# Kernel optimization log

Hardware: AMD Instinct MI355X
Metric: run time of the kernel (lower is better)

## Reference

```python
import jax, jax.numpy as jnp
import numpy as np

B, D = 8192, 1024
HR, HE, HF = 512, 4096, 2048
N_OPS, N_TASKS = 4, 4

def setup_inputs() -> dict:
    key = jax.random.key(0)
    ks = jax.random.split(key, 20)
    s = 0.02
    return {
        "x":        jax.random.normal(ks[0], (B, D), jnp.float32),
        # router
        "W_r1":   s*jax.random.normal(ks[1], (D, HR), jnp.float32),
        "b_r1":     jnp.zeros((HR,), jnp.float32),
        "W_dom":  s*jax.random.normal(ks[2], (HR, 2), jnp.float32),
        "b_dom":    jnp.zeros((2,), jnp.float32),
        "W_mop":  s*jax.random.normal(ks[3], (HR, N_OPS), jnp.float32),
        "W_lt":   s*jax.random.normal(ks[4], (HR, N_TASKS), jnp.float32),
        # math expert (operation hint = additive embedding)
        "op_emb": s*jax.random.normal(ks[5], (N_OPS, D), jnp.float32),
        "W_m1":   s*jax.random.normal(ks[6], (D, HE), jnp.float32),
        "b_m1":     jnp.zeros((HE,), jnp.float32),
        "W_m2":   s*jax.random.normal(ks[7], (HE, D), jnp.float32),
        "b_m2":     jnp.zeros((D,), jnp.float32),
        # language expert (task hint = additive embedding)
        "task_emb": s*jax.random.normal(ks[8], (N_TASKS, D), jnp.float32),
        "W_l1":   s*jax.random.normal(ks[9], (D, HE), jnp.float32),
        "b_l1":     jnp.zeros((HE,), jnp.float32),
        "W_l2":   s*jax.random.normal(ks[10], (HE, D), jnp.float32),
        "b_l2":     jnp.zeros((D,), jnp.float32),
        # fusion
        "W_f1":   s*jax.random.normal(ks[11], (D, HF), jnp.float32),
        "b_f1":     jnp.zeros((HF,), jnp.float32),
        "W_f2":   s*jax.random.normal(ks[12], (HF, D), jnp.float32),
        "b_f2":     jnp.zeros((D,), jnp.float32),
    }

def reference(x, W_r1, b_r1, W_dom, b_dom, W_mop, W_lt,
              op_emb, W_m1, b_m1, W_m2, b_m2,
              task_emb, W_l1, b_l1, W_l2, b_l2,
              W_f1, b_f1, W_f2, b_f2):
    # --- router ---
    h = jax.nn.relu(x @ W_r1 + b_r1)                      # [B, HR]
    dom_logits = h @ W_dom + b_dom                        # [B, 2]
    expert_weights = jax.nn.softmax(dom_logits, axis=-1)  # [B, 2]
    primary = jnp.argmax(dom_logits, axis=-1)             # [B]
    math_op = jnp.argmax(h @ W_mop, axis=-1)              # [B]
    lang_task = jnp.argmax(h @ W_lt, axis=-1)             # [B]
    # --- experts (vectorized equivalent of per-sample dispatch) ---
    math_in = x + op_emb[math_op]                         # [B, D]
    math_out = jax.nn.relu(math_in @ W_m1 + b_m1) @ W_m2 + b_m2
    lang_in = x + task_emb[lang_task]                     # [B, D]
    lang_out = jax.nn.relu(lang_in @ W_l1 + b_l1) @ W_l2 + b_l2
    selected = jnp.where((primary == 0)[:, None], math_out, lang_out)  # [B, D]
    # --- fusion: scale by routing weight of the chosen expert + MLP residual ---
    w = jnp.take_along_axis(expert_weights, primary[:, None], axis=1)  # [B, 1]
    fused = w * selected
    final = fused + jax.nn.relu(fused @ W_f1 + b_f1) @ W_f2 + b_f2     # [B, D]
    return final
```

## Files before the change

kernel.cpp:

```cpp
#include <hip/hip_runtime.h>
#include <hip/hip_bf16.h>
#include <stdint.h>

#define NB 8192
#define DD 1024
#define HRD 512
#define HED 4096
#define HFD 2048

typedef __attribute__((ext_vector_type(8))) short bf16x8;
typedef __attribute__((ext_vector_type(4))) float f32x4;
typedef unsigned short u16;

__device__ __forceinline__ u16 f2b(float f) {
    union { float f; uint32_t i; } c; c.f = f;
    uint32_t r = c.i + 0x7FFF + ((c.i >> 16) & 1);
    return (u16)(r >> 16);
}
__device__ __forceinline__ float b2f(u16 u) {
    union { uint32_t i; float f; } c; c.i = ((uint32_t)u) << 16; return c.f;
}

__device__ __forceinline__ void xcd_swz(int flat, int nwg, int nFast, int& f, int& s) {
    int xcd = flat & 7, rest = flat >> 3;
    int q = nwg >> 3, r = nwg & 7;
    int wg = (xcd < r ? xcd * (q + 1) : r * (q + 1) + (xcd - r) * q) + rest;
    f = wg % nFast; s = wg / nFast;
}

#define GLDS(g, l) __builtin_amdgcn_global_load_lds( \
    (const __attribute__((address_space(1))) void*)(g), \
    (__attribute__((address_space(3))) void*)(l), 16, 0, 0)

__global__ void k_init(int* cnt) { if (threadIdx.x < 2) cnt[threadIdx.x] = 0; }

__global__ __launch_bounds__(256) void k_split(const float4* __restrict__ x4,
                                               ushort4* __restrict__ hi4,
                                               ushort4* __restrict__ lo4) {
    int i = blockIdx.x * 256 + threadIdx.x;
    float4 v = x4[i];
    ushort4 h, l;
    h.x = f2b(v.x); l.x = f2b(v.x - b2f(h.x));
    h.y = f2b(v.y); l.y = f2b(v.y - b2f(h.y));
    h.z = f2b(v.z); l.z = f2b(v.z - b2f(h.z));
    h.w = f2b(v.w); l.w = f2b(v.w - b2f(h.w));
    hi4[i] = h; lo4[i] = l;
}

__global__ __launch_bounds__(256) void k_transpose(const float* __restrict__ in,
                                                   u16* __restrict__ out, int R, int C) {
    __shared__ float s[64][65];
    int tx = threadIdx.x & 63, ty = threadIdx.x >> 6;
    int c0 = blockIdx.x * 64, r0 = blockIdx.y * 64;
#pragma unroll
    for (int j = 0; j < 16; j++) { int r = ty + j * 4; s[r][tx] = in[(size_t)(r0 + r) * C + c0 + tx]; }
    __syncthreads();
#pragma unroll
    for (int j = 0; j < 16; j++) { int c = ty + j * 4; out[(size_t)(c0 + c) * R + r0 + tx] = f2b(s[tx][c]); }
}

__global__ __launch_bounds__(256) void k_transpose_split(const float* __restrict__ in,
                                                         u16* __restrict__ ohi, u16* __restrict__ olo,
                                                         int R, int C) {
    __shared__ float s[64][65];
    int tx = threadIdx.x & 63, ty = threadIdx.x >> 6;
    int c0 = blockIdx.x * 64, r0 = blockIdx.y * 64;
#pragma unroll
    for (int j = 0; j < 16; j++) { int r = ty + j * 4; s[r][tx] = in[(size_t)(r0 + r) * C + c0 + tx]; }
    __syncthreads();
#pragma unroll
    for (int j = 0; j < 16; j++) {
        int c = ty + j * 4;
        float v = s[tx][c];
        u16 h = f2b(v);
        ohi[(size_t)(c0 + c) * R + r0 + tx] = h;
        olo[(size_t)(c0 + c) * R + r0 + tx] = f2b(v - b2f(h));
    }
}

__device__ __forceinline__ void stage_tile(const char* gRowBase, long rowStrideBytes,
                                           u16* s, int tid) {
    int wave = tid >> 6, lane = tid & 63;
#pragma unroll
    for (int is = 0; is < 4; ++is) {
        int c = wave * 4 + is;
        int row = c * 8 + (lane >> 3);
        const char* g = gRowBase + (long)row * rowStrideBytes + (lane & 7) * 16;
        GLDS(g, (char*)s + c * 1024);
    }
}

__global__ __launch_bounds__(256) void k_router(const u16* __restrict__ Ah, const u16* __restrict__ Al,
                                                const u16* __restrict__ Bh, const u16* __restrict__ Bl,
                                                const float* __restrict__ bias, float* __restrict__ H) {
    __shared__ u16 sAh[2][128 * 64], sAl[2][128 * 64], sBh[2][128 * 64], sBl[2][128 * 64];
    int tid = threadIdx.x, lane = tid & 63, wave = tid >> 6;
    int flat = blockIdx.y * gridDim.x + blockIdx.x;
    int bm, bn;
    xcd_swz(flat, gridDim.x * gridDim.y, gridDim.y, bn, bm);
    f32x4 acc[4][4];
#pragma unroll
    for (int i = 0; i < 4; i++)
#pragma unroll
        for (int j = 0; j < 4; j++) acc[i][j] = (f32x4)0.f;
    int wm = (wave & 1) * 64, wn = (wave >> 1) * 64;
    const char* ahBase = (const char*)(Ah + (size_t)bm * 128 * DD);
    const char* alBase = (const char*)(Al + (size_t)bm * 128 * DD);
    const char* bhBase = (const char*)(Bh + (size_t)bn * 128 * DD);
    const char* blBase = (const char*)(Bl + (size_t)bn * 128 * DD);
    const int nk = DD / 64;
    stage_tile(ahBase, DD * 2, sAh[0], tid);
    stage_tile(alBase, DD * 2, sAl[0], tid);
    stage_tile(bhBase, DD * 2, sBh[0], tid);
    stage_tile(blBase, DD * 2, sBl[0], tid);
    asm volatile("s_waitcnt vmcnt(0)" ::: "memory");
    __builtin_amdgcn_s_barrier();
    int cur = 0;
    for (int it = 0; it < nk; ++it) {
        if (it + 1 < nk) {
            size_t ofs = (size_t)(it + 1) * 128;
            stage_tile(ahBase + ofs, DD * 2, sAh[cur ^ 1], tid);
            stage_tile(alBase + ofs, DD * 2, sAl[cur ^ 1], tid);
            stage_tile(bhBase + ofs, DD * 2, sBh[cur ^ 1], tid);
            stage_tile(blBase + ofs, DD * 2, sBl[cur ^ 1], tid);
        }
        const u16* pAh = sAh[cur]; const u16* pAl = sAl[cur];
        const u16* pBh = sBh[cur]; const u16* pBl = sBl[cur];
#pragma unroll
        for (int kk = 0; kk < 2; kk++) {
            int kofs = kk * 64 + (lane >> 4) * 16;
            bf16x8 vbh[4], vbl[4];
#pragma unroll
            for (int ni = 0; ni < 4; ni++) {
                int rB = (wn + ni * 16 + (lane & 15)) * 128 + kofs;
                vbh[ni] = *(const bf16x8*)((const char*)pBh + rB);
                vbl[ni] = *(const bf16x8*)((const char*)pBl + rB);
            }
#pragma unroll
            for (int mi = 0; mi < 4; mi++) {
                int rA = (wm + mi * 16 + (lane & 15)) * 128 + kofs;
                bf16x8 vah = *(const bf16x8*)((const char*)pAh + rA);
                bf16x8 val = *(const bf16x8*)((const char*)pAl + rA);
#pragma unroll
                for (int ni = 0; ni < 4; ni++) {
                    acc[mi][ni] = __builtin_amdgcn_mfma_f32_16x16x32_bf16(vah, vbh[ni], acc[mi][ni], 0, 0, 0);
                    acc[mi][ni] = __builtin_amdgcn_mfma_f32_16x16x32_bf16(vah, vbl[ni], acc[mi][ni], 0, 0, 0);
                    acc[mi][ni] = __builtin_amdgcn_mfma_f32_16x16x32_bf16(val, vbh[ni], acc[mi][ni], 0, 0, 0);
                }
            }
        }
        asm volatile("s_waitcnt vmcnt(0)" ::: "memory");
        __builtin_amdgcn_s_barrier();
        cur ^= 1;
    }
    int quad = lane >> 4, cl = lane & 15;
#pragma unroll
    for (int mi = 0; mi < 4; mi++)
#pragma unroll
        for (int r = 0; r < 4; r++) {
            int row = bm * 128 + wm + mi * 16 + quad * 4 + r;
#pragma unroll
            for (int ni = 0; ni < 4; ni++) {
                int col = bn * 128 + wn + ni * 16 + cl;
                float v = acc[mi][ni][r] + bias[col];
                H[(size_t)row * HRD + col] = fmaxf(v, 0.f);
            }
        }
}

__global__ __launch_bounds__(256) void k_heads(const float* __restrict__ H,
                                               const float* __restrict__ Wd, const float* __restrict__ bd,
                                               const float* __restrict__ Wm, const float* __restrict__ Wl,
                                               int* __restrict__ cnt, int* __restrict__ perm,
                                               float* __restrict__ wsc, int* __restrict__ eic) {
    int lane = threadIdx.x & 63, wave = threadIdx.x >> 6;
    int r = blockIdx.x * 4 + wave;
    const float4* h4 = (const float4*)(H + (size_t)r * HRD);
    float4 v0 = h4[lane * 2], v1 = h4[lane * 2 + 1];
    float hv[8] = {v0.x, v0.y, v0.z, v0.w, v1.x, v1.y, v1.z, v1.w};
    float a[10];
#pragma unroll
    for (int t = 0; t < 10; t++) a[t] = 0.f;
    int kbase = lane * 8;
#pragma unroll
    for (int j = 0; j < 8; j++) {
        int k = kbase + j;
        float h_ = hv[j];
        float2 wd = ((const float2*)Wd)[k];
        a[0] += h_ * wd.x; a[1] += h_ * wd.y;
        float4 wm = ((const float4*)Wm)[k];
        a[2] += h_ * wm.x; a[3] += h_ * wm.y; a[4] += h_ * wm.z; a[5] += h_ * wm.w;
        float4 wl = ((const float4*)Wl)[k];
        a[6] += h_ * wl.x; a[7] += h_ * wl.y; a[8] += h_ * wl.z; a[9] += h_ * wl.w;
    }
#pragma unroll
    for (int t = 0; t < 10; t++)
#pragma unroll
        for (int off = 32; off > 0; off >>= 1) a[t] += __shfl_down(a[t], off);
    if (lane == 0) {
        float d0 = a[0] + bd[0], d1 = a[1] + bd[1];
        int primary = (d1 > d0) ? 1 : 0;
        float w = 1.f / (1.f + expf(-fabsf(d0 - d1)));
        int mi = 0; float mv = a[2];
        if (a[3] > mv) { mv = a[3]; mi = 1; }
        if (a[4] > mv) { mv = a[4]; mi = 2; }
        if (a[5] > mv) { mv = a[5]; mi = 3; }
        int li = 0; float lv = a[6];
        if (a[7] > lv) { lv = a[7]; li = 1; }
        if (a[8] > lv) { lv = a[8]; li = 2; }
        int pos;
        if (a[9] > lv) { lv = a[9]; li = 3; }
        if (primary == 0) pos = atomicAdd(&cnt[0], 1);
        else              pos = NB - 1 - atomicAdd(&cnt[1], 1);
        perm[pos] = r; wsc[pos] = w; eic[pos] = (primary == 0) ? mi : li;
    }
}

__global__ __launch_bounds__(256) void k_gather(const float* __restrict__ x,
                                                const float* __restrict__ op_emb,
                                                const float* __restrict__ task_emb,
                                                const int* __restrict__ perm, const int* __restrict__ eic,
                                                const int* __restrict__ cnt, u16* __restrict__ xin) {
    int lane = threadIdx.x & 63, wave = threadIdx.x >> 6;
    int i = blockIdx.x * 4 + wave;
    int n0 = cnt[0];
    int r = perm[i];
    const float* emb = ((i >= n0) ? task_emb : op_emb) + (size_t)eic[i] * DD;
    const float4* x4 = (const float4*)(x + (size_t)r * DD);
    const float4* e4 = (const float4*)emb;
    ushort4* o4 = (ushort4*)(xin + (size_t)i * DD);
#pragma unroll
    for (int j = 0; j < 4; j++) {
        int idx = lane + j * 64;
        float4 xv = x4[idx], ev = e4[idx];
        ushort4 o;
        o.x = f2b(xv.x + ev.x); o.y = f2b(xv.y + ev.y);
        o.z = f2b(xv.z + ev.z); o.w = f2b(xv.w + ev.w);
        o4[idx] = o;
    }
}

template <bool DUAL>
__global__ __launch_bounds__(512) void k_g256(
    const u16* __restrict__ A, const u16* __restrict__ B0w, const u16* __restrict__ B1w,
    const float* __restrict__ bias0, const float* __restrict__ bias1,
    u16* __restrict__ Out, int K, int N, const int* __restrict__ cnt) {
    __shared__ __align__(16) u16 sA[2][256 * 64];
    __shared__ __align__(16) u16 sB[2][256 * 64];
    const int tid = threadIdx.x, lane = tid & 63, wave = tid >> 6;
    int flat = blockIdx.y * gridDim.x + blockIdx.x;
    int t, bn;
    xcd_swz(flat, gridDim.x * gridDim.y, gridDim.y, bn, t);

    int tile = t, storeLo = 0, storeHi = 0x7fffffff;
    const u16* Bt = B0w; const float* bias = bias0;
    if constexpr (DUAL) {
        int n0 = cnt[0];
        int tb = n0 >> 8;
        bool isMath = (t <= tb) && (t < NB / 256);
        tile = isMath ? t : (t - 1);
        if (isMath) { storeLo = tile * 256; storeHi = n0 < storeLo + 256 ? n0 : storeLo + 256; }
        else        { storeHi = tile * 256 + 256; storeLo = n0 > tile * 256 ? n0 : tile * 256;
                      Bt = B1w; bias = bias1; }
        if (storeLo >= storeHi) return;
    }

    f32x4 acc[8][4];
#pragma unroll
    for (int i = 0; i < 8; i++)
#pragma unroll
        for (int j = 0; j < 4; j++) acc[i][j] = (f32x4)0.f;

    const int wm = (wave & 1) * 128;
    const int wn = (wave >> 1) * 64;
    const int rl = lane & 15, q = lane >> 4, x7 = lane & 7;
    const int aRow = (wave & 1) * 64;
    const int bRow = (wave >> 1) * 32;

    const long stride = (long)K * 2;
    const char* aBase = (const char*)A + (size_t)tile * 256 * stride;
    const char* bBase = (const char*)Bt + (size_t)bn * 256 * stride;
    const long srcOfs = (long)((lane & 7) ^ (lane >> 3)) << 4;
    const int waveOfs = wave * 1024;
    const int l8 = lane >> 3;

    auto SH_A = [&](int h, int kt, int d) {
        long kofs = (long)kt * 128 + srcOfs;
#pragma unroll
        for (int i = 0; i < 2; i++) {
            int gr = wave * 8 + l8 + h * 64 + i * 128;
            GLDS(aBase + (long)gr * stride + kofs,
                 (char*)&sA[d][0] + h * 16384 + i * 8192 + waveOfs);
        }
    };
    auto SH_B = [&](int h, int kt, int d) {
        long kofs = (long)kt * 128 + srcOfs;
#pragma unroll
        for (int i = 0; i < 2; i++) {
            int rp = i * 64 + wave * 8 + l8;
            int gn = (rp & 31) + ((rp >> 5) << 6) + h * 32;
            GLDS(bBase + (long)gn * stride + kofs,
                 (char*)&sB[d][0] + h * 16384 + i * 8192 + waveOfs);
        }
    };

    const int nk = K >> 6;
    SH_A(0, 0, 0); SH_B(0, 0, 0); SH_B(1, 0, 0); SH_A(1, 0, 0);
    if (nk > 1) {
        SH_A(0, 1, 1); SH_B(0, 1, 1); SH_B(1, 1, 1);
        asm volatile("s_waitcnt vmcnt(6)" ::: "memory");
    } else {
        asm volatile("s_waitcnt vmcnt(0)" ::: "memory");
    }
    __builtin_amdgcn_s_barrier();

    bf16x8 va[4][2], vb0[2][2], vb1[2][2];
    for (int kt = 0; kt < nk; ++kt) {
        const int cur = kt & 1;
        const char* pA = (const char*)&sA[cur][0];
        const char* pB = (const char*)&sB[cur][0];
#pragma unroll
        for (int f = 0; f < 4; f++)
#pragma unroll
            for (int kk = 0; kk < 2; kk++)
                va[f][kk] = *(const bf16x8*)(pA + (aRow + f * 16 + rl) * 128 + (((kk * 4 + q) ^ x7) << 4));
#pragma unroll
        for (int g = 0; g < 2; g++)
#pragma unroll
            for (int kk = 0; kk < 2; kk++)
                vb0[g][kk] = *(const bf16x8*)(pB + (bRow + g * 16 + rl) * 128 + (((kk * 4 + q) ^ x7) << 4));
        if (kt + 1 < nk) SH_A(1, kt + 1, cur ^ 1);
        __builtin_amdgcn_s_setprio(1);
#pragma unroll
        for (int f = 0; f < 4; f++)
#pragma unroll
            for (int g = 0; g < 2; g++)
#pragma unroll
                for (int kk = 0; kk < 2; kk++)
                    acc[f][g] = __builtin_amdgcn_mfma_f32_16x16x32_bf16(va[f][kk], vb0[g][kk], acc[f][g], 0, 0, 0);
        __builtin_amdgcn_s_setprio(0);
        asm volatile("" ::: "memory");
        __builtin_amdgcn_s_barrier();
#pragma unroll
        for (int g = 0; g < 2; g++)
#pragma unroll
            for (int kk = 0; kk < 2; kk++)
                vb1[g][kk] = *(const bf16x8*)(pB + (bRow + 128 + g * 16 + rl) * 128 + (((kk * 4 + q) ^ x7) << 4));
        if (kt + 2 < nk) SH_B(0, kt + 2, cur);
        __builtin_amdgcn_s_setprio(1);
#pragma unroll
        for (int f = 0; f < 4; f++)
#pragma unroll
            for (int g = 0; g < 2; g++)
#pragma unroll
                for (int kk = 0; kk < 2; kk++)
                    acc[f][2 + g] = __builtin_amdgcn_mfma_f32_16x16x32_bf16(va[f][kk], vb1[g][kk], acc[f][2 + g], 0, 0, 0);
        __builtin_amdgcn_s_setprio(0);
        asm volatile("" ::: "memory");
        __builtin_amdgcn_s_barrier();
#pragma unroll
        for (int f = 0; f < 4; f++)
#pragma unroll
            for (int kk = 0; kk < 2; kk++)
                va[f][kk] = *(const bf16x8*)(pA + (aRow + 128 + f * 16 + rl) * 128 + (((kk * 4 + q) ^ x7) << 4));
        if (kt + 2 < nk) SH_B(1, kt + 2, cur);
        __builtin_amdgcn_s_setprio(1);
#pragma unroll
        for (int f = 0; f < 4; f++)
#pragma unroll
            for (int g = 0; g < 2; g++)
#pragma unroll
                for (int kk = 0; kk < 2; kk++)
                    acc[4 + f][2 + g] = __builtin_amdgcn_mfma_f32_16x16x32_bf16(va[f][kk], vb1[g][kk], acc[4 + f][2 + g], 0, 0, 0);
        __builtin_amdgcn_s_setprio(0);
        asm volatile("" ::: "memory");
        __builtin_amdgcn_s_barrier();
        if (kt + 2 < nk) {
            SH_A(0, kt + 2, cur);
            asm volatile("s_waitcnt vmcnt(6)" ::: "memory");
        } else {
            asm volatile("s_waitcnt vmcnt(0)" ::: "memory");
        }
        __builtin_amdgcn_s_setprio(1);
#pragma unroll
        for (int f = 0; f < 4; f++)
#pragma unroll
            for (int g = 0; g < 2; g++)
#pragma unroll
                for (int kk = 0; kk < 2; kk++)
                    acc[4 + f][g] = __builtin_amdgcn_mfma_f32_16x16x32_bf16(va[f][kk], vb0[g][kk], acc[4 + f][g], 0, 0, 0);
        __builtin_amdgcn_s_setprio(0);
        asm volatile("" ::: "memory");
        __builtin_amdgcn_s_barrier();
    }

    const int quad = lane >> 4, cl = lane & 15;
#pragma unroll
    for (int f = 0; f < 8; f++)
#pragma unroll
        for (int rr = 0; rr < 4; rr++) {
            int grow = tile * 256 + wm + ((f & 3) * 16) + ((f >> 2) * 64) + quad * 4 + rr;
            if constexpr (DUAL) { if (grow < storeLo || grow >= storeHi) continue; }
#pragma unroll
            for (int g = 0; g < 4; g++) {
                int col = bn * 256 + wn + ((g & 1) * 16) + ((g >> 1) * 32) + cl;
                float v = acc[f][g][rr] + bias[col];
                Out[(size_t)grow * N + col] = f2b(fmaxf(v, 0.f));
            }
        }
}

template <int EPI, bool DUAL>
__global__ __launch_bounds__(512) void k_gemm8p(
    const u16* __restrict__ A, const u16* __restrict__ B0, const u16* __restrict__ B1,
    const float* __restrict__ bias0, const float* __restrict__ bias1,
    void* __restrict__ Out, int K, int N,
    const int* __restrict__ cnt, const float* __restrict__ wsel,
    const int* __restrict__ perm, const u16* __restrict__ resid) {
    __shared__ __align__(16) u16 sA[2][128 * 64];
    __shared__ __align__(16) u16 sB[2][128 * 64];
    const int tid = threadIdx.x, lane = tid & 63, wave = tid >> 6;
    int flat = blockIdx.y * gridDim.x + blockIdx.x;
    int t, bn;
    xcd_swz(flat, gridDim.x * gridDim.y, gridDim.y, bn, t);

    int n0 = 0, tile = t, storeLo = 0, storeHi = 0x7fffffff;
    const u16* Bt = B0; const float* bias = bias0;
    if constexpr (DUAL) {
        n0 = cnt[0];
        int tb = n0 >> 7;
        bool isMath = (t <= tb) && (t < 64);
        tile = isMath ? t : (t - 1);
        if (isMath) { storeLo = tile * 128; storeHi = n0 < storeLo + 128 ? n0 : storeLo + 128; }
        else        { storeHi = tile * 128 + 128; storeLo = n0 > tile * 128 ? n0 : tile * 128;
                      Bt = B1; bias = bias1; }
        if (storeLo >= storeHi) return;
    }

    f32x4 acc[4][2];
#pragma unroll
    for (int i = 0; i < 4; i++)
#pragma unroll
        for (int j = 0; j < 2; j++) acc[i][j] = (f32x4)0.f;

    const int wm = (wave & 1) * 64;
    const int wn = (wave >> 1) * 32;
    const int rl = lane & 15, q = lane >> 4, x7 = lane & 7;

    const long stride = (long)K * 2;
    const char* aBase = (const char*)A + (size_t)tile * 128 * stride;
    const char* bBase = (const char*)Bt + (size_t)bn * 128 * stride;
    const int rowInUnit = tid >> 3;
    const long srcOfs = (long)((tid & 7) ^ (rowInUnit & 7)) << 4;
    const int ldsWaveOfs = wave * 1024;

    auto STAGE = [&](int kt, int d) {
        long kofs = (long)kt * 128 + srcOfs;
#pragma unroll
        for (int i = 0; i < 2; i++)
            GLDS(aBase + (long)(i * 64 + rowInUnit) * stride + kofs,
                 (char*)&sA[d][0] + i * 8192 + ldsWaveOfs);
#pragma unroll
        for (int i = 0; i < 2; i++)
            GLDS(bBase + (long)(i * 64 + rowInUnit) * stride + kofs,
                 (char*)&sB[d][0] + i * 8192 + ldsWaveOfs);
    };

    STAGE(0, 0);
    const int nk = K >> 6;
    for (int k = 0; k < nk; ++k) {
        const int r_ = k & 1;
        if (k + 1 < nk) {
            STAGE(k + 1, r_ ^ 1);
            asm volatile("s_waitcnt vmcnt(4)" ::: "memory");
        } else {
            asm volatile("s_waitcnt vmcnt(0)" ::: "memory");
        }
        __builtin_amdgcn_s_barrier();
        const char* pA = (const char*)&sA[r_][0];
        const char* pB = (const char*)&sB[r_][0];
        bf16x8 vaA[2][2], vaB[2][2], vb0[2], vb1[2];
#pragma unroll
        for (int f = 0; f < 2; f++)
#pragma unroll
            for (int kk = 0; kk < 2; kk++)
                vaA[f][kk] = *(const bf16x8*)(pA + (wm + f * 16 + rl) * 128 + (((kk * 4 + q) ^ x7) << 4));
#pragma unroll
        for (int kk = 0; kk < 2; kk++)
            vb0[kk] = *(const bf16x8*)(pB + (wn + rl) * 128 + (((kk * 4 + q) ^ x7) << 4));
        __builtin_amdgcn_s_setprio(1);
#pragma unroll
        for (int f = 0; f < 2; f++)
#pragma unroll
            for (int kk = 0; kk < 2; kk++)
                acc[f][0] = __builtin_amdgcn_mfma_f32_16x16x32_bf16(vaA[f][kk], vb0[kk], acc[f][0], 0, 0, 0);
        __builtin_amdgcn_s_setprio(0);
#pragma unroll
        for (int kk = 0; kk < 2; kk++)
            vb1[kk] = *(const bf16x8*)(pB + (wn + 16 + rl) * 128 + (((kk * 4 + q) ^ x7) << 4));
        __builtin_amdgcn_s_setprio(1);
#pragma unroll
        for (int f = 0; f < 2; f++)
#pragma unroll
            for (int kk = 0; kk < 2; kk++)
                acc[f][1] = __builtin_amdgcn_mfma_f32_16x16x32_bf16(vaA[f][kk], vb1[kk], acc[f][1], 0, 0, 0);
        __builtin_amdgcn_s_setprio(0);
#pragma unroll
        for (int f = 0; f < 2; f++)
#pragma unroll
            for (int kk = 0; kk < 2; kk++)
                vaB[f][kk] = *(const bf16x8*)(pA + (wm + 32 + f * 16 + rl) * 128 + (((kk * 4 + q) ^ x7) << 4));
        __builtin_amdgcn_s_setprio(1);
#pragma unroll
        for (int f = 0; f < 2; f++)
#pragma unroll
            for (int kk = 0; kk < 2; kk++)
                acc[2 + f][1] = __builtin_amdgcn_mfma_f32_16x16x32_bf16(vaB[f][kk], vb1[kk], acc[2 + f][1], 0, 0, 0);
        __builtin_amdgcn_s_setprio(0);
        __builtin_amdgcn_s_setprio(1);
#pragma unroll
        for (int f = 0; f < 2; f++)
#pragma unroll
            for (int kk = 0; kk < 2; kk++)
                acc[2 + f][0] = __builtin_amdgcn_mfma_f32_16x16x32_bf16(vaB[f][kk], vb0[kk], acc[2 + f][0], 0, 0, 0);
        __builtin_amdgcn_s_setprio(0);
        asm volatile("" ::: "memory");
        __builtin_amdgcn_s_barrier();
    }

    const int quad = lane >> 4, cl = lane & 15;
#pragma unroll
    for (int mi = 0; mi < 4; mi++)
#pragma unroll
        for (int r = 0; r < 4; r++) {
            int grow = tile * 128 + wm + mi * 16 + quad * 4 + r;
            if constexpr (DUAL) { if (grow < storeLo || grow >= storeHi) continue; }
#pragma unroll
            for (int ni = 0; ni < 2; ni++) {
                int col = bn * 128 + wn + ni * 16 + cl;
                float v = acc[mi][ni][r] + bias[col];
                if constexpr (EPI == 0) {
                    ((u16*)Out)[(size_t)grow * N + col] = f2b(fmaxf(v, 0.f));
                } else if constexpr (EPI == 1) {
                    ((u16*)Out)[(size_t)grow * N + col] = f2b(v * wsel[grow]);
                } else {
                    v += b2f(resid[(size_t)grow * N + col]);
                    ((float*)Out)[(size_t)perm[grow] * N + col] = v;
                }
            }
        }
}

extern "C" void kernel_launch(void* const* d_in, const int* in_sizes, int n_in,
                              void* d_out, int out_size, void* d_ws, size_t ws_size,
                              hipStream_t stream) {
    const float* x      = (const float*)d_in[0];
    const float* W_r1   = (const float*)d_in[1];
    const float* b_r1   = (const float*)d_in[2];
    const float* W_dom  = (const float*)d_in[3];
    const float* b_dom  = (const float*)d_in[4];
    const float* W_mop  = (const float*)d_in[5];
    const float* W_lt   = (const float*)d_in[6];
    const float* op_emb = (const float*)d_in[7];
    const float* W_m1   = (const float*)d_in[8];
    const float* b_m1   = (const float*)d_in[9];
    const float* W_m2   = (const float*)d_in[10];
    const float* b_m2   = (const float*)d_in[11];
    const float* task_emb = (const float*)d_in[12];
    const float* W_l1   = (const float*)d_in[13];
    const float* b_l1   = (const float*)d_in[14];
    const float* W_l2   = (const float*)d_in[15];
    const float* b_l2   = (const float*)d_in[16];
    const float* W_f1   = (const float*)d_in[17];
    const float* b_f1   = (const float*)d_in[18];
    const float* W_f2   = (const float*)d_in[19];
    const float* b_f2   = (const float*)d_in[20];

    char* wsp = (char*)d_ws;
    size_t off = 0;
    auto take = [&](size_t bytes) -> char* {
        char* p = wsp + off;
        off += (bytes + 255) & ~(size_t)255;
        return p;
    };
    u16* Wr_hi = (u16*)take((size_t)HRD * DD * 2);
    u16* Wr_lo = (u16*)take((size_t)HRD * DD * 2);
    u16* Wm1t  = (u16*)take((size_t)HED * DD * 2);
    u16* Wl1t  = (u16*)take((size_t)HED * DD * 2);
    u16* Wm2t  = (u16*)take((size_t)DD * HED * 2);
    u16* Wl2t  = (u16*)take((size_t)DD * HED * 2);
    u16* Wf1t  = (u16*)take((size_t)HFD * DD * 2);
    u16* Wf2t  = (u16*)take((size_t)DD * HFD * 2);
    u16* x_hi  = (u16*)take((size_t)NB * DD * 2);
    u16* x_lo  = (u16*)take((size_t)NB * DD * 2);
    float* Hbuf = (float*)take((size_t)NB * HRD * 4);
    u16* hid   = (u16*)take((size_t)NB * HED * 2);
    int* cnt   = (int*)take(256);
    int* perm  = (int*)take(NB * 4);
    int* eic   = (int*)take(NB * 4);
    float* wsc = (float*)take(NB * 4);
    u16* xin   = x_hi;
    u16* fused = x_lo;
    u16* hid2  = Wm1t;

    k_init<<<1, 64, 0, stream>>>(cnt);
    k_split<<<(NB * DD / 4) / 256, 256, 0, stream>>>((const float4*)x, (ushort4*)x_hi, (ushort4*)x_lo);
    k_transpose_split<<<dim3(HRD / 64, DD / 64), 256, 0, stream>>>(W_r1, Wr_hi, Wr_lo, DD, HRD);
    k_transpose<<<dim3(HED / 64, DD / 64), 256, 0, stream>>>(W_m1, Wm1t, DD, HED);
    k_transpose<<<dim3(HED / 64, DD / 64), 256, 0, stream>>>(W_l1, Wl1t, DD, HED);
    k_transpose<<<dim3(DD / 64, HED / 64), 256, 0, stream>>>(W_m2, Wm2t, HED, DD);
    k_transpose<<<dim3(DD / 64, HED / 64), 256, 0, stream>>>(W_l2, Wl2t, HED, DD);
    k_transpose<<<dim3(HFD / 64, DD / 64), 256, 0, stream>>>(W_f1, Wf1t, DD, HFD);
    k_transpose<<<dim3(DD / 64, HFD / 64), 256, 0, stream>>>(W_f2, Wf2t, HFD, DD);

    k_router<<<dim3(NB / 128, HRD / 128), 256, 0, stream>>>(x_hi, x_lo, Wr_hi, Wr_lo, b_r1, Hbuf);
    k_heads<<<NB / 4, 256, 0, stream>>>(Hbuf, W_dom, b_dom, W_mop, W_lt, cnt, perm, wsc, eic);
    k_gather<<<NB / 4, 256, 0, stream>>>(x, op_emb, task_emb, perm, eic, cnt, xin);

    k_g256<true><<<dim3(NB / 256 + 1, HED / 256), 512, 0, stream>>>(
        xin, Wm1t, Wl1t, b_m1, b_l1, hid, DD, HED, cnt);
    k_gemm8p<1, true><<<dim3(NB / 128 + 1, DD / 128), 512, 0, stream>>>(
        hid, Wm2t, Wl2t, b_m2, b_l2, fused, HED, DD, cnt, wsc, nullptr, nullptr);
    k_g256<false><<<dim3(NB / 256, HFD / 256), 512, 0, stream>>>(
        fused, Wf1t, nullptr, b_f1, nullptr, hid2, DD, HFD, cnt);
    k_gemm8p<2, false><<<dim3(NB / 128, DD / 128), 512, 0, stream>>>(
        hid2, Wf2t, nullptr, b_f2, nullptr, d_out, HFD, DD, cnt, nullptr, perm, fused);
}
```

Baseline: 647.6 us.

## Use 256x128 tiles with staggered half-tile prefetch in down-projection GEMMs

Replaces the 128x128 double-buffered GEMM used for the expert down-projection and the fusion second layer with a 256x128 tile kernel. Global-to-LDS loads are split into A and B halves and issued between the four MFMA phases of each k-step, with barriers between phases. The aim is more reuse per B load and better overlap of memory traffic with matrix math. In exchange it uses more LDS and accumulator registers and launches half as many workgroups, which may lower occupancy and leave fewer blocks to spread across CUs.

```diff
diff --git a/kernel.cpp b/kernel.cpp
--- a/kernel.cpp
+++ b/kernel.cpp
@@ -411,118 +411,141 @@
 }
 
 template <int EPI, bool DUAL>
-__global__ __launch_bounds__(512) void k_gemm8p(
+__global__ __launch_bounds__(512) void k_gSTAG(
     const u16* __restrict__ A, const u16* __restrict__ B0, const u16* __restrict__ B1,
     const float* __restrict__ bias0, const float* __restrict__ bias1,
     void* __restrict__ Out, int K, int N,
     const int* __restrict__ cnt, const float* __restrict__ wsel,
     const int* __restrict__ perm, const u16* __restrict__ resid) {
-    __shared__ __align__(16) u16 sA[2][128 * 64];
+    __shared__ __align__(16) u16 sA[2][256 * 64];
     __shared__ __align__(16) u16 sB[2][128 * 64];
     const int tid = threadIdx.x, lane = tid & 63, wave = tid >> 6;
     int flat = blockIdx.y * gridDim.x + blockIdx.x;
     int t, bn;
     xcd_swz(flat, gridDim.x * gridDim.y, gridDim.y, bn, t);
 
-    int n0 = 0, tile = t, storeLo = 0, storeHi = 0x7fffffff;
+    int tile = t, storeLo = 0, storeHi = 0x7fffffff;
     const u16* Bt = B0; const float* bias = bias0;
     if constexpr (DUAL) {
-        n0 = cnt[0];
-        int tb = n0 >> 7;
-        bool isMath = (t <= tb) && (t < 64);
+        int n0 = cnt[0];
+        int tb = n0 >> 8;
+        bool isMath = (t <= tb) && (t < NB / 256);
         tile = isMath ? t : (t - 1);
-        if (isMath) { storeLo = tile * 128; storeHi = n0 < storeLo + 128 ? n0 : storeLo + 128; }
-        else        { storeHi = tile * 128 + 128; storeLo = n0 > tile * 128 ? n0 : tile * 128;
+        if (isMath) { storeLo = tile * 256; storeHi = n0 < storeLo + 256 ? n0 : storeLo + 256; }
+        else        { storeHi = tile * 256 + 256; storeLo = n0 > tile * 256 ? n0 : tile * 256;
                       Bt = B1; bias = bias1; }
         if (storeLo >= storeHi) return;
     }
 
-    f32x4 acc[4][2];
-#pragma unroll
-    for (int i = 0; i < 4; i++)
+    f32x4 acc[8][2];
+#pragma unroll
+    for (int i = 0; i < 8; i++)
 #pragma unroll
         for (int j = 0; j < 2; j++) acc[i][j] = (f32x4)0.f;
 
-    const int wm = (wave & 1) * 64;
+    const int wm = (wave & 1) * 128;
     const int wn = (wave >> 1) * 32;
     const int rl = lane & 15, q = lane >> 4, x7 = lane & 7;
+    const int aRow = (wave & 1) * 64;
+    const int bRow = (wave >> 1) * 16;
 
     const long stride = (long)K * 2;
-    const char* aBase = (const char*)A + (size_t)tile * 128 * stride;
+    const char* aBase = (const char*)A + (size_t)tile * 256 * stride;
     const char* bBase = (const char*)Bt + (size_t)bn * 128 * stride;
-    const int rowInUnit = tid >> 3;
-    const long srcOfs = (long)((tid & 7) ^ (rowInUnit & 7)) << 4;
-    const int ldsWaveOfs = wave * 1024;
-
-    auto STAGE = [&](int kt, int d) {
+    const long srcOfs = (long)((lane & 7) ^ (lane >> 3)) << 4;
+    const int waveOfs = wave * 1024;
+    const int l8 = lane >> 3;
+
+    auto SH_A = [&](int h, int kt, int d) {
         long kofs = (long)kt * 128 + srcOfs;
 #pragma unroll
-        for (int i = 0; i < 2; i++)
-            GLDS(aBase + (long)(i * 64 + rowInUnit) * stride + kofs,
-                 (char*)&sA[d][0] + i * 8192 + ldsWaveOfs);
-#pragma unroll
-        for (int i = 0; i < 2; i++)
-            GLDS(bBase + (long)(i * 64 + rowInUnit) * stride + kofs,
-                 (char*)&sB[d][0] + i * 8192 + ldsWaveOfs);
+        for (int i = 0; i < 2; i++) {
+            int gr = wave * 8 + l8 + h * 64 + i * 128;
+            GLDS(aBase + (long)gr * stride + kofs,
+                 (char*)&sA[d][0] + h * 16384 + i * 8192 + waveOfs);
+        }
     };
-
-    STAGE(0, 0);
+    auto SH_B = [&](int h, int kt, int d) {
+        long kofs = (long)kt * 128 + srcOfs;
+        int rp = wave * 8 + l8;
+        int gn = (rp & 15) + ((rp >> 4) << 5) + h * 16;
+        GLDS(bBase + (long)gn * stride + kofs,
+             (char*)&sB[d][0] + h * 8192 + waveOfs);
+    };
+
     const int nk = K >> 6;
-    for (int k = 0; k < nk; ++k) {
-        const int r_ = k & 1;
-        if (k + 1 < nk) {
-            STAGE(k + 1, r_ ^ 1);
+    SH_A(0, 0, 0); SH_B(0, 0, 0); SH_B(1, 0, 0); SH_A(1, 0, 0);
+    if (nk > 1) {
+        SH_A(0, 1, 1); SH_B(0, 1, 1); SH_B(1, 1, 1);
+        asm volatile("s_waitcnt vmcnt(4)" ::: "memory");
+    } else {
+        asm volatile("s_waitcnt vmcnt(0)" ::: "memory");
+    }
+    __builtin_amdgcn_s_barrier();
+
+    bf16x8 va[4][2], vb0[2], vb1[2];
+    for (int kt = 0; kt < nk; ++kt) {
+        const int cur = kt & 1;
+        const char* pA = (const char*)&sA[cur][0];
+        const char* pB = (const char*)&sB[cur][0];
+#pragma unroll
+        for (int f = 0; f < 4; f++)
+#pragma unroll
+            for (int kk = 0; kk < 2; kk++)
+                va[f][kk] = *(const bf16x8*)(pA + (aRow + f * 16 + rl) * 128 + (((kk * 4 + q) ^ x7) << 4));
+#pragma unroll
+        for (int kk = 0; kk < 2; kk++)
+            vb0[kk] = *(const bf16x8*)(pB + (bRow + rl) * 128 + (((kk * 4 + q) ^ x7) << 4));
+        if (kt + 1 < nk) SH_A(1, kt + 1, cur ^ 1);
+        __builtin_amdgcn_s_setprio(1);
+#pragma unroll
+        for (int f = 0; f < 4; f++)
+#pragma unroll
+            for (int kk = 0; kk < 2; kk++)
+                acc[f][0] = __builtin_amdgcn_mfma_f32_16x16x32_bf16(va[f][kk], vb0[kk], acc[f][0], 0, 0, 0);
+        __builtin_amdgcn_s_setprio(0);
+        asm volatile("" ::: "memory");
+        __builtin_amdgcn_s_barrier();
+#pragma unroll
+        for (int kk = 0; kk < 2; kk++)
+            vb1[kk] = *(const bf16x8*)(pB + (64 + bRow + rl) * 128 + (((kk * 4 + q) ^ x7) << 4));
+        if (kt + 2 < nk) SH_B(0, kt + 2, cur);
+        __builtin_amdgcn_s_setprio(1);
+#pragma unroll
+        for (int f = 0; f < 4; f++)
+#pragma unroll
+            for (int kk = 0; kk < 2; kk++)
+                acc[f][1] = __builtin_amdgcn_mfma_f32_16x16x32_bf16(va[f][kk], vb1[kk], acc[f][1], 0, 0, 0);
+        __builtin_amdgcn_s_setprio(0);
+        asm volatile("" ::: "memory");
+        __builtin_amdgcn_s_barrier();
+#pragma unroll
+        for (int f = 0; f < 4; f++)
+#pragma unroll
+            for (int kk = 0; kk < 2; kk++)
+                va[f][kk] = *(const bf16x8*)(pA + (aRow + 128 + f * 16 + rl) * 128 + (((kk * 4 + q) ^ x7) << 4));
+        if (kt + 2 < nk) SH_B(1, kt + 2, cur);
+        __builtin_amdgcn_s_setprio(1);
+#pragma unroll
+        for (int f = 0; f < 4; f++)
+#pragma unroll
+            for (int kk = 0; kk < 2; kk++)
+                acc[4 + f][1] = __builtin_amdgcn_mfma_f32_16x16x32_bf16(va[f][kk], vb1[kk], acc[4 + f][1], 0, 0, 0);
+        __builtin_amdgcn_s_setprio(0);
+        asm volatile("" ::: "memory");
+        __builtin_amdgcn_s_barrier();
+        if (kt + 2 < nk) {
+            SH_A(0, kt + 2, cur);
             asm volatile("s_waitcnt vmcnt(4)" ::: "memory");
         } else {
             asm volatile("s_waitcnt vmcnt(0)" ::: "memory");
         }
-        __builtin_amdgcn_s_barrier();
-        const char* pA = (const char*)&sA[r_][0];
-        const char* pB = (const char*)&sB[r_][0];
-        bf16x8 vaA[2][2], vaB[2][2], vb0[2], vb1[2];
-#pragma unroll
-        for (int f = 0; f < 2; f++)
-#pragma unroll
-            for (int kk = 0; kk < 2; kk++)
-                vaA[f][kk] = *(const bf16x8*)(pA + (wm + f * 16 + rl) * 128 + (((kk * 4 + q) ^ x7) << 4));
-#pragma unroll
-        for (int kk = 0; kk < 2; kk++)
-            vb0[kk] = *(const bf16x8*)(pB + (wn + rl) * 128 + (((kk * 4 + q) ^ x7) << 4));
-        __builtin_amdgcn_s_setprio(1);
-#pragma unroll
-        for (int f = 0; f < 2; f++)
-#pragma unroll
-            for (int kk = 0; kk < 2; kk++)
-                acc[f][0] = __builtin_amdgcn_mfma_f32_16x16x32_bf16(vaA[f][kk], vb0[kk], acc[f][0], 0, 0, 0);
-        __builtin_amdgcn_s_setprio(0);
-#pragma unroll
-        for (int kk = 0; kk < 2; kk++)
-            vb1[kk] = *(const bf16x8*)(pB + (wn + 16 + rl) * 128 + (((kk * 4 + q) ^ x7) << 4));
-        __builtin_amdgcn_s_setprio(1);
-#pragma unroll
-        for (int f = 0; f < 2; f++)
-#pragma unroll
-            for (int kk = 0; kk < 2; kk++)
-                acc[f][1] = __builtin_amdgcn_mfma_f32_16x16x32_bf16(vaA[f][kk], vb1[kk], acc[f][1], 0, 0, 0);
-        __builtin_amdgcn_s_setprio(0);
-#pragma unroll
-        for (int f = 0; f < 2; f++)
-#pragma unroll
-            for (int kk = 0; kk < 2; kk++)
-                vaB[f][kk] = *(const bf16x8*)(pA + (wm + 32 + f * 16 + rl) * 128 + (((kk * 4 + q) ^ x7) << 4));
-        __builtin_amdgcn_s_setprio(1);
-#pragma unroll
-        for (int f = 0; f < 2; f++)
-#pragma unroll
-            for (int kk = 0; kk < 2; kk++)
-                acc[2 + f][1] = __builtin_amdgcn_mfma_f32_16x16x32_bf16(vaB[f][kk], vb1[kk], acc[2 + f][1], 0, 0, 0);
-        __builtin_amdgcn_s_setprio(0);
-        __builtin_amdgcn_s_setprio(1);
-#pragma unroll
-        for (int f = 0; f < 2; f++)
-#pragma unroll
-            for (int kk = 0; kk < 2; kk++)
-                acc[2 + f][0] = __builtin_amdgcn_mfma_f32_16x16x32_bf16(vaB[f][kk], vb0[kk], acc[2 + f][0], 0, 0, 0);
+        __builtin_amdgcn_s_setprio(1);
+#pragma unroll
+        for (int f = 0; f < 4; f++)
+#pragma unroll
+            for (int kk = 0; kk < 2; kk++)
+                acc[4 + f][0] = __builtin_amdgcn_mfma_f32_16x16x32_bf16(va[f][kk], vb0[kk], acc[4 + f][0], 0, 0, 0);
         __builtin_amdgcn_s_setprio(0);
         asm volatile("" ::: "memory");
         __builtin_amdgcn_s_barrier();
@@ -530,18 +553,16 @@
 
     const int quad = lane >> 4, cl = lane & 15;
 #pragma unroll
-    for (int mi = 0; mi < 4; mi++)
-#pragma unroll
-        for (int r = 0; r < 4; r++) {
-            int grow = tile * 128 + wm + mi * 16 + quad * 4 + r;
+    for (int f = 0; f < 8; f++)
+#pragma unroll
+        for (int rr = 0; rr < 4; rr++) {
+            int grow = tile * 256 + wm + ((f & 3) * 16) + ((f >> 2) * 64) + quad * 4 + rr;
             if constexpr (DUAL) { if (grow < storeLo || grow >= storeHi) continue; }
 #pragma unroll
-            for (int ni = 0; ni < 2; ni++) {
-                int col = bn * 128 + wn + ni * 16 + cl;
-                float v = acc[mi][ni][r] + bias[col];
-                if constexpr (EPI == 0) {
-                    ((u16*)Out)[(size_t)grow * N + col] = f2b(fmaxf(v, 0.f));
-                } else if constexpr (EPI == 1) {
+            for (int g = 0; g < 2; g++) {
+                int col = bn * 128 + wn + g * 16 + cl;
+                float v = acc[f][g][rr] + bias[col];
+                if constexpr (EPI == 1) {
                     ((u16*)Out)[(size_t)grow * N + col] = f2b(v * wsel[grow]);
                 } else {
                     v += b2f(resid[(size_t)grow * N + col]);
@@ -619,10 +640,10 @@
 
     k_g256<true><<<dim3(NB / 256 + 1, HED / 256), 512, 0, stream>>>(
         xin, Wm1t, Wl1t, b_m1, b_l1, hid, DD, HED, cnt);
-    k_gemm8p<1, true><<<dim3(NB / 128 + 1, DD / 128), 512, 0, stream>>>(
+    k_gSTAG<1, true><<<dim3(NB / 256 + 1, DD / 128), 512, 0, stream>>>(
         hid, Wm2t, Wl2t, b_m2, b_l2, fused, HED, DD, cnt, wsc, nullptr, nullptr);
     k_g256<false><<<dim3(NB / 256, HFD / 256), 512, 0, stream>>>(
         fused, Wf1t, nullptr, b_f1, nullptr, hid2, DD, HFD, cnt);
-    k_gemm8p<2, false><<<dim3(NB / 128, DD / 128), 512, 0, stream>>>(
+    k_gSTAG<2, false><<<dim3(NB / 256, DD / 128), 512, 0, stream>>>(
         hid2, Wf2t, nullptr, b_f2, nullptr, d_out, HFD, DD, cnt, nullptr, perm, fused);
 }
```

After: 672.1 us. 1.04x slower.
